# Kernel optimization log

Hardware: AMD Instinct MI355X
Metric: run time of the kernel (lower is better)

## Reference

```python
import jax, jax.numpy as jnp
import numpy as np

N = 8192       # batch_size
D = 128        # embedding dim
C = 1000       # num classes
EPS = 1e-8     # torch CosineSimilarity eps


def setup_inputs() -> dict:
    key = jax.random.key(0)
    k1, k2, k3, k4 = jax.random.split(key, 4)
    inst_embed = jax.random.normal(k1, (N, D), dtype=jnp.float32)
    proxy = jax.random.normal(k2, (N, D), dtype=jnp.float32)
    # binary mask marking same-class (non-negative) pairs, stored as float
    negative_mask = (jax.random.uniform(k3, (N, C)) < 0.5).astype(jnp.float32)
    labels = jax.random.randint(k4, (N,), 0, C)
    temperature = jnp.float32(0.07)
    margin = jnp.float32(0.0)
    return {
        'inst_embed': inst_embed,
        'proxy': proxy,
        'negative_mask': negative_mask,
        'labels': labels,
        'temperature': temperature,
        'margin': margin,
    }


def _remove_diag(M):
    # M: [h, h] -> [h, h-1], dropping the diagonal, row-major order (as torch bool-mask view)
    h = M.shape[0]
    j = jnp.arange(h - 1)[None, :]
    i = jnp.arange(h)[:, None]
    cols = j + (j >= i)  # skip column i in row i
    return jnp.take_along_axis(M, cols, axis=1)


def _l2_normalize(x):
    return x / jnp.maximum(jnp.linalg.norm(x, axis=-1, keepdims=True), EPS)


def reference(inst_embed, proxy, negative_mask, labels, temperature, margin):
    negative_mask = negative_mask.T                       # [C, N]
    xn = _l2_normalize(inst_embed)                        # [N, D]
    sim = xn @ xn.T                                       # [N, N] cosine similarity matrix
    instance_zone = jnp.exp((_remove_diag(sim) - margin) / temperature)  # [N, N-1]
    pn = _l2_normalize(proxy)
    inst2proxy_positive = jnp.exp((jnp.sum(xn * pn, axis=-1) - margin) / temperature)  # [N]
    # pos_collected_numerator == True branch
    mask_4_remove_negatives = _remove_diag(negative_mask[labels])        # [N, N-1]
    inst2inst_positives = instance_zone * mask_4_remove_negatives
    numerator = inst2proxy_positive + inst2inst_positives.sum(axis=1)
    denominator = inst2proxy_positive + instance_zone.sum(axis=1)
    criterion = -jnp.log(temperature * (numerator / denominator)).mean()
    return criterion
```

## Files before the change

kernel.cpp:

```cpp
#include <hip/hip_runtime.h>
#include <hip/hip_bf16.h>

typedef unsigned short u16;
typedef unsigned int   u32;
typedef unsigned long long u64;
typedef __attribute__((ext_vector_type(8))) short short8;
typedef __attribute__((ext_vector_type(4))) float float4v;

#define N 8192
#define D 128
#define C 1000
#define TILE 128
#define LDT 136
#define NW64 (N / 64)
#define JQ 8
#define JW (JQ * 2)
#define LOG2E 1.44269504088896340736f

__global__ void norm_kernel(const float* __restrict__ x, const float* __restrict__ pr,
                            u16* __restrict__ xnb, float* __restrict__ p_out,
                            float* __restrict__ den, float* __restrict__ num,
                            const float* __restrict__ tp, const float* __restrict__ mp) {
    const int wave = threadIdx.x >> 6;
    const int lane = threadIdx.x & 63;
    const int row  = blockIdx.x * 4 + wave;

    const float2* xr  = (const float2*)(x  + (size_t)row * D);
    const float2* prr = (const float2*)(pr + (size_t)row * D);
    float2 xv = xr[lane];
    float2 pv = prr[lane];

    float sx  = xv.x * xv.x + xv.y * xv.y;
    float sp  = pv.x * pv.x + pv.y * pv.y;
    float sxp = xv.x * pv.x + xv.y * pv.y;
    #pragma unroll
    for (int off = 32; off; off >>= 1) {
        sx  += __shfl_xor(sx,  off);
        sp  += __shfl_xor(sp,  off);
        sxp += __shfl_xor(sxp, off);
    }
    float nx = fmaxf(sqrtf(sx), 1e-8f);
    float np = fmaxf(sqrtf(sp), 1e-8f);
    float inv = 1.0f / nx;

    __hip_bfloat16 b0 = __float2bfloat16(xv.x * inv);
    __hip_bfloat16 b1 = __float2bfloat16(xv.y * inv);
    ((__hip_bfloat162*)xnb)[(size_t)row * 64 + lane] = __halves2bfloat162(b0, b1);

    if (lane == 0) {
        float T = tp[0], M = mp[0];
        p_out[row] = __expf((sxp / (nx * np) - M) / T);
        den[row] = 0.0f;
        num[row] = 0.0f;
    }
}

__global__ void pack_kernel(const float* __restrict__ nm, u64* __restrict__ packed) {
    __shared__ u32 Ls[64 * 65];
    const int lane = threadIdx.x & 63;
    const int wv   = threadIdx.x >> 6;
    const int jt   = blockIdx.x;
    const int lt   = blockIdx.y;
    const int j0   = jt * 64;
    const int l    = lt * 64 + lane;
    const bool lv  = l < C;

    #pragma unroll
    for (int rr = 0; rr < 16; rr++) {
        const int r = wv * 16 + rr;
        float v = lv ? nm[(size_t)(j0 + r) * C + l] : 0.0f;
        Ls[r * 65 + lane] = (v > 0.5f) ? 1u : 0u;
    }
    __syncthreads();
    #pragma unroll
    for (int cc = 0; cc < 16; cc++) {
        const int c = wv * 16 + cc;
        u64 m = __ballot(Ls[lane * 65 + c] != 0u);
        if (lane == 0 && (lt * 64 + c) < C)
            packed[(size_t)(lt * 64 + c) * NW64 + jt] = m;
    }
}

template <bool DIAG>
__device__ __forceinline__ void epilogue(const float4v acc[4][4], const u64* __restrict__ Ms,
                                         float dacc[4][4], float nacc[4][4],
                                         int wr, int wc, int kq, int m0,
                                         int ibase, int jbase, int q,
                                         float kA2, float kB2) {
    #pragma unroll
    for (int tm = 0; tm < 4; tm++) {
        #pragma unroll
        for (int r = 0; r < 4; r++) {
            const int lrow = wr * 64 + tm * 16 + kq * 4 + r;
            const u64 ws = Ms[lrow * JW + q * 2 + wc] >> m0;
            const u32 wlo = (u32)ws, whi = (u32)(ws >> 32);
            const int gi = ibase + lrow;
            #pragma unroll
            for (int tn = 0; tn < 4; tn++) {
                float e = __builtin_amdgcn_exp2f(fmaf(acc[tm][tn][r], kA2, kB2));
                if (DIAG) {
                    const int gj = jbase + wc * 64 + tn * 16 + m0;
                    if (gi == gj) e = 0.0f;
                }
                dacc[tm][r] += e;
                const u32 bit = ((tn < 2) ? (wlo >> (tn * 16)) : (whi >> ((tn - 2) * 16))) & 1u;
                nacc[tm][r] = fmaf((float)bit, e, nacc[tm][r]);
            }
        }
    }
}

__global__ __launch_bounds__(256, 2)
void cc_main(const u16* __restrict__ xnb, const int* __restrict__ labels,
             const u64* __restrict__ packed,
             float* __restrict__ den, float* __restrict__ num,
             const float* __restrict__ tp, const float* __restrict__ mp) {
    __shared__ u16 As[TILE * LDT];
    __shared__ u64 Ms[TILE * JW];

    const int tid  = threadIdx.x;
    const int lane = tid & 63;
    const int wv   = tid >> 6;
    const int wr   = wv >> 1;
    const int wc   = wv & 1;
    const int m0   = lane & 15;
    const int kq   = lane >> 4;
    const int ibase  = blockIdx.x * TILE;
    const int jsplit = blockIdx.y;
    const int jt0    = jsplit * JQ;

    const float T = tp[0];
    const float M = mp[0];
    const float kA2 = LOG2E / T;
    const float kB2 = -M * LOG2E / T;

    {
        const int r = tid >> 1, h = tid & 1;
        const uint4* src = (const uint4*)(xnb + (size_t)(ibase + r) * D + h * 64);
        uint4* dst = (uint4*)(As + r * LDT + h * 64);
        #pragma unroll
        for (int qq = 0; qq < 8; qq++) dst[qq] = src[qq];
    }
    #pragma unroll
    for (int t = 0; t < 8; t++) {
        const int idx = t * 256 + tid;
        const int row = idx >> 4, h = idx & 15;
        const int lab = labels[ibase + row];
        Ms[idx] = packed[(size_t)lab * NW64 + jt0 * 2 + h];
    }
    __syncthreads();

    float dacc[4][4] = {};
    float nacc[4][4] = {};

    const u16* Abase = As + (wr * 64 + m0) * LDT + kq * 8;
    const u16* Blane = xnb + (size_t)(wc * 64 + m0) * D + kq * 8;

    short8 bc[4], bn[4];
    {
        const u16* Bp = Blane + (size_t)(jt0 * TILE) * D;
        #pragma unroll
        for (int tn = 0; tn < 4; tn++) bc[tn] = *(const short8*)(Bp + tn * (16 * D));
    }

    for (int q = 0; q < JQ; q++) {
        const int jt = jt0 + q;
        const int jbase = jt * TILE;
        const u16* Bq = Blane + (size_t)jbase * D;

        float4v acc[4][4];
        #pragma unroll
        for (int a = 0; a < 4; a++)
            #pragma unroll
            for (int b = 0; b < 4; b++)
                acc[a][b] = (float4v){0.f, 0.f, 0.f, 0.f};

        #pragma unroll
        for (int kk = 0; kk < 4; kk++) {
            if (kk < 3) {
                #pragma unroll
                for (int tn = 0; tn < 4; tn++)
                    bn[tn] = *(const short8*)(Bq + tn * (16 * D) + (kk + 1) * 32);
            } else if (q < JQ - 1) {
                const u16* Bnq = Bq + (size_t)TILE * D;
                #pragma unroll
                for (int tn = 0; tn < 4; tn++)
                    bn[tn] = *(const short8*)(Bnq + tn * (16 * D));
            }
            short8 a_f[4];
            #pragma unroll
            for (int tm = 0; tm < 4; tm++)
                a_f[tm] = *(const short8*)(Abase + tm * (16 * LDT) + kk * 32);
            #pragma unroll
            for (int tm = 0; tm < 4; tm++)
                #pragma unroll
                for (int tn = 0; tn < 4; tn++)
                    acc[tm][tn] = __builtin_amdgcn_mfma_f32_16x16x32_bf16(
                        a_f[tm], bc[tn], acc[tm][tn], 0, 0, 0);
            #pragma unroll
            for (int tn = 0; tn < 4; tn++) bc[tn] = bn[tn];
        }

        if (jt == blockIdx.x)
            epilogue<true >(acc, Ms, dacc, nacc, wr, wc, kq, m0, ibase, jbase, q, kA2, kB2);
        else
            epilogue<false>(acc, Ms, dacc, nacc, wr, wc, kq, m0, ibase, jbase, q, kA2, kB2);
    }

    #pragma unroll
    for (int tm = 0; tm < 4; tm++) {
        #pragma unroll
        for (int r = 0; r < 4; r++) {
            float d = dacc[tm][r], n = nacc[tm][r];
            #pragma unroll
            for (int off = 1; off < 16; off <<= 1) {
                d += __shfl_xor(d, off);
                n += __shfl_xor(n, off);
            }
            if (m0 == 0) {
                const int gi = ibase + wr * 64 + tm * 16 + kq * 4 + r;
                atomicAdd(&den[gi], d);
                atomicAdd(&num[gi], n);
            }
        }
    }
}

__global__ void loss_kernel(const float* __restrict__ p, const float* __restrict__ den,
                            const float* __restrict__ num, float* __restrict__ out,
                            const float* __restrict__ tp) {
    __shared__ float red[16];
    const float T = tp[0];
    float s = 0.0f;
    #pragma unroll
    for (int t = 0; t < N / 1024; t++) {
        const int i = t * 1024 + threadIdx.x;
        float pi = p[i];
        s += -__logf(T * (pi + num[i]) / (pi + den[i]));
    }
    #pragma unroll
    for (int off = 32; off; off >>= 1) s += __shfl_xor(s, off);
    const int lane = threadIdx.x & 63, wv = threadIdx.x >> 6;
    if (lane == 0) red[wv] = s;
    __syncthreads();
    if (wv == 0) {
        float t = (lane < 16) ? red[lane] : 0.0f;
        #pragma unroll
        for (int off = 8; off; off >>= 1) t += __shfl_xor(t, off);
        if (lane == 0) out[0] = t / (float)N;
    }
}

extern "C" void kernel_launch(void* const* d_in, const int* in_sizes, int n_in,
                              void* d_out, int out_size, void* d_ws, size_t ws_size,
                              hipStream_t stream) {
    (void)in_sizes; (void)n_in; (void)out_size; (void)ws_size;
    const float* inst   = (const float*)d_in[0];
    const float* proxy  = (const float*)d_in[1];
    const float* nm     = (const float*)d_in[2];
    const int*   labels = (const int*)d_in[3];
    const float* temp   = (const float*)d_in[4];
    const float* marg   = (const float*)d_in[5];
    float* out = (float*)d_out;

    char* ws = (char*)d_ws;
    u16*   xnb    = (u16*)ws;
    float* p_arr  = (float*)(ws + 2097152);
    u64*   packed = (u64*)(ws + 2129920);
    float* den    = (float*)(ws + 3153920);
    float* num    = (float*)(ws + 3186688);

    pack_kernel<<<dim3(N / 64, 16), 256, 0, stream>>>(nm, packed);
    norm_kernel<<<N / 4, 256, 0, stream>>>(inst, proxy, xnb, p_arr, den, num, temp, marg);
    cc_main<<<dim3(N / TILE, 8), 256, 0, stream>>>(xnb, labels, packed, den, num, temp, marg);
    loss_kernel<<<1, 1024, 0, stream>>>(p_arr, den, num, out, temp);
}
```

Before: 142.4 us.

## Fuse prep kernels, fold loss into main kernel via last-block counter, vectorize epilogue

Merges the mask-packing and normalization kernels into one launch split by block index. The separate loss kernel is removed: the last cc_main block to finish, found with an atomic counter, computes the final reduction. The epilogue now works on float4 vectors per row group so the exp and accumulate steps can issue as packed operations. Together these cut launch overhead and the tail launch, at the cost of an atomic counter, a threadfence in every block, and a serial reduction done by one block.

```diff
diff --git a/kernel.cpp b/kernel.cpp
--- a/kernel.cpp
+++ b/kernel.cpp
@@ -15,97 +15,113 @@
 #define NW64 (N / 64)
 #define JQ 8
 #define JW (JQ * 2)
+#define NBLK (64 * 8)
 #define LOG2E 1.44269504088896340736f
 
-__global__ void norm_kernel(const float* __restrict__ x, const float* __restrict__ pr,
+__global__ void prep_kernel(const float* __restrict__ nm, u64* __restrict__ packed,
+                            const float* __restrict__ x, const float* __restrict__ pr,
                             u16* __restrict__ xnb, float* __restrict__ p_out,
                             float* __restrict__ den, float* __restrict__ num,
+                            u32* __restrict__ counter,
                             const float* __restrict__ tp, const float* __restrict__ mp) {
-    const int wave = threadIdx.x >> 6;
-    const int lane = threadIdx.x & 63;
-    const int row  = blockIdx.x * 4 + wave;
-
-    const float2* xr  = (const float2*)(x  + (size_t)row * D);
-    const float2* prr = (const float2*)(pr + (size_t)row * D);
-    float2 xv = xr[lane];
-    float2 pv = prr[lane];
-
-    float sx  = xv.x * xv.x + xv.y * xv.y;
-    float sp  = pv.x * pv.x + pv.y * pv.y;
-    float sxp = xv.x * pv.x + xv.y * pv.y;
-    #pragma unroll
-    for (int off = 32; off; off >>= 1) {
-        sx  += __shfl_xor(sx,  off);
-        sp  += __shfl_xor(sp,  off);
-        sxp += __shfl_xor(sxp, off);
-    }
-    float nx = fmaxf(sqrtf(sx), 1e-8f);
-    float np = fmaxf(sqrtf(sp), 1e-8f);
-    float inv = 1.0f / nx;
-
-    __hip_bfloat16 b0 = __float2bfloat16(xv.x * inv);
-    __hip_bfloat16 b1 = __float2bfloat16(xv.y * inv);
-    ((__hip_bfloat162*)xnb)[(size_t)row * 64 + lane] = __halves2bfloat162(b0, b1);
-
-    if (lane == 0) {
-        float T = tp[0], M = mp[0];
-        p_out[row] = __expf((sxp / (nx * np) - M) / T);
-        den[row] = 0.0f;
-        num[row] = 0.0f;
-    }
-}
-
-__global__ void pack_kernel(const float* __restrict__ nm, u64* __restrict__ packed) {
     __shared__ u32 Ls[64 * 65];
+    const int bid  = blockIdx.x;
     const int lane = threadIdx.x & 63;
     const int wv   = threadIdx.x >> 6;
-    const int jt   = blockIdx.x;
-    const int lt   = blockIdx.y;
-    const int j0   = jt * 64;
-    const int l    = lt * 64 + lane;
-    const bool lv  = l < C;
-
-    #pragma unroll
-    for (int rr = 0; rr < 16; rr++) {
-        const int r = wv * 16 + rr;
-        float v = lv ? nm[(size_t)(j0 + r) * C + l] : 0.0f;
-        Ls[r * 65 + lane] = (v > 0.5f) ? 1u : 0u;
-    }
-    __syncthreads();
-    #pragma unroll
-    for (int cc = 0; cc < 16; cc++) {
-        const int c = wv * 16 + cc;
-        u64 m = __ballot(Ls[lane * 65 + c] != 0u);
-        if (lane == 0 && (lt * 64 + c) < C)
-            packed[(size_t)(lt * 64 + c) * NW64 + jt] = m;
+
+    if (bid < 2048) {
+        const int jt = bid & 127;
+        const int lt = bid >> 7;
+        const int j0 = jt * 64;
+        const int l  = lt * 64 + lane;
+        const bool lv = l < C;
+        if (bid == 0 && threadIdx.x == 0) counter[0] = 0u;
+
+        #pragma unroll
+        for (int rr = 0; rr < 16; rr++) {
+            const int r = wv * 16 + rr;
+            float v = lv ? nm[(size_t)(j0 + r) * C + l] : 0.0f;
+            Ls[r * 65 + lane] = (v > 0.5f) ? 1u : 0u;
+        }
+        __syncthreads();
+        #pragma unroll
+        for (int cc = 0; cc < 16; cc++) {
+            const int c = wv * 16 + cc;
+            u64 m = __ballot(Ls[lane * 65 + c] != 0u);
+            if (lane == 0 && (lt * 64 + c) < C)
+                packed[(size_t)(lt * 64 + c) * NW64 + jt] = m;
+        }
+    } else {
+        const int row = (bid - 2048) * 4 + wv;
+        const float2* xr  = (const float2*)(x  + (size_t)row * D);
+        const float2* prr = (const float2*)(pr + (size_t)row * D);
+        float2 xv = xr[lane];
+        float2 pv = prr[lane];
+
+        float sx  = xv.x * xv.x + xv.y * xv.y;
+        float sp  = pv.x * pv.x + pv.y * pv.y;
+        float sxp = xv.x * pv.x + xv.y * pv.y;
+        #pragma unroll
+        for (int off = 32; off; off >>= 1) {
+            sx  += __shfl_xor(sx,  off);
+            sp  += __shfl_xor(sp,  off);
+            sxp += __shfl_xor(sxp, off);
+        }
+        float nx = fmaxf(sqrtf(sx), 1e-8f);
+        float np = fmaxf(sqrtf(sp), 1e-8f);
+        float inv = 1.0f / nx;
+
+        __hip_bfloat16 b0 = __float2bfloat16(xv.x * inv);
+        __hip_bfloat16 b1 = __float2bfloat16(xv.y * inv);
+        ((__hip_bfloat162*)xnb)[(size_t)row * 64 + lane] = __halves2bfloat162(b0, b1);
+
+        if (lane == 0) {
+            float T = tp[0], M = mp[0];
+            p_out[row] = __expf((sxp / (nx * np) - M) / T);
+            den[row] = 0.0f;
+            num[row] = 0.0f;
+        }
     }
 }
 
 template <bool DIAG>
 __device__ __forceinline__ void epilogue(const float4v acc[4][4], const u64* __restrict__ Ms,
-                                         float dacc[4][4], float nacc[4][4],
+                                         float4v dacc[4], float4v nacc[4],
                                          int wr, int wc, int kq, int m0,
                                          int ibase, int jbase, int q,
                                          float kA2, float kB2) {
     #pragma unroll
     for (int tm = 0; tm < 4; tm++) {
+        u32 lo[4], hi[4];
         #pragma unroll
         for (int r = 0; r < 4; r++) {
             const int lrow = wr * 64 + tm * 16 + kq * 4 + r;
-            const u64 ws = Ms[lrow * JW + q * 2 + wc] >> m0;
-            const u32 wlo = (u32)ws, whi = (u32)(ws >> 32);
-            const int gi = ibase + lrow;
-            #pragma unroll
-            for (int tn = 0; tn < 4; tn++) {
-                float e = __builtin_amdgcn_exp2f(fmaf(acc[tm][tn][r], kA2, kB2));
-                if (DIAG) {
-                    const int gj = jbase + wc * 64 + tn * 16 + m0;
-                    if (gi == gj) e = 0.0f;
+            const u64 w = Ms[lrow * JW + q * 2 + wc];
+            lo[r] = (u32)(w >> m0);
+            hi[r] = (u32)(w >> (m0 + 32));
+        }
+        #pragma unroll
+        for (int tn = 0; tn < 4; tn++) {
+            float4v t = acc[tm][tn] * kA2 + kB2;
+            float4v e;
+            #pragma unroll
+            for (int r = 0; r < 4; r++) e[r] = __builtin_amdgcn_exp2f(t[r]);
+            if (DIAG) {
+                const int gj = jbase + wc * 64 + tn * 16 + m0;
+                #pragma unroll
+                for (int r = 0; r < 4; r++) {
+                    const int gi = ibase + wr * 64 + tm * 16 + kq * 4 + r;
+                    if (gi == gj) e[r] = 0.0f;
                 }
-                dacc[tm][r] += e;
-                const u32 bit = ((tn < 2) ? (wlo >> (tn * 16)) : (whi >> ((tn - 2) * 16))) & 1u;
-                nacc[tm][r] = fmaf((float)bit, e, nacc[tm][r]);
-            }
+            }
+            dacc[tm] += e;
+            float4v mf;
+            #pragma unroll
+            for (int r = 0; r < 4; r++) {
+                const u32 bit = ((tn < 2) ? (lo[r] >> (tn * 16)) : (hi[r] >> ((tn - 2) * 16))) & 1u;
+                mf[r] = (float)bit;
+            }
+            nacc[tm] += mf * e;
         }
     }
 }
@@ -114,9 +130,13 @@
 void cc_main(const u16* __restrict__ xnb, const int* __restrict__ labels,
              const u64* __restrict__ packed,
              float* __restrict__ den, float* __restrict__ num,
+             const float* __restrict__ p_arr, u32* __restrict__ counter,
+             float* __restrict__ out,
              const float* __restrict__ tp, const float* __restrict__ mp) {
     __shared__ u16 As[TILE * LDT];
     __shared__ u64 Ms[TILE * JW];
+    __shared__ u32 done_s;
+    __shared__ float red[4];
 
     const int tid  = threadIdx.x;
     const int lane = tid & 63;
@@ -150,8 +170,8 @@
     }
     __syncthreads();
 
-    float dacc[4][4] = {};
-    float nacc[4][4] = {};
+    float4v dacc[4] = {};
+    float4v nacc[4] = {};
 
     const u16* Abase = As + (wr * 64 + m0) * LDT + kq * 8;
     const u16* Blane = xnb + (size_t)(wc * 64 + m0) * D + kq * 8;
@@ -224,30 +244,30 @@
             }
         }
     }
-}
-
-__global__ void loss_kernel(const float* __restrict__ p, const float* __restrict__ den,
-                            const float* __restrict__ num, float* __restrict__ out,
-                            const float* __restrict__ tp) {
-    __shared__ float red[16];
-    const float T = tp[0];
-    float s = 0.0f;
-    #pragma unroll
-    for (int t = 0; t < N / 1024; t++) {
-        const int i = t * 1024 + threadIdx.x;
-        float pi = p[i];
-        s += -__logf(T * (pi + num[i]) / (pi + den[i]));
-    }
-    #pragma unroll
-    for (int off = 32; off; off >>= 1) s += __shfl_xor(s, off);
-    const int lane = threadIdx.x & 63, wv = threadIdx.x >> 6;
-    if (lane == 0) red[wv] = s;
+
+    __threadfence();
+    if (tid == 0) done_s = atomicAdd(counter, 1u);
     __syncthreads();
-    if (wv == 0) {
-        float t = (lane < 16) ? red[lane] : 0.0f;
-        #pragma unroll
-        for (int off = 8; off; off >>= 1) t += __shfl_xor(t, off);
-        if (lane == 0) out[0] = t / (float)N;
+    if (done_s == NBLK - 1) {
+        float s = 0.0f;
+        #pragma unroll
+        for (int t = 0; t < N / 256; t++) {
+            const int i = t * 256 + tid;
+            float dv = __hip_atomic_load(&den[i], __ATOMIC_RELAXED, __HIP_MEMORY_SCOPE_AGENT);
+            float nv = __hip_atomic_load(&num[i], __ATOMIC_RELAXED, __HIP_MEMORY_SCOPE_AGENT);
+            float pi = p_arr[i];
+            s += -__logf(T * (pi + nv) / (pi + dv));
+        }
+        #pragma unroll
+        for (int off = 32; off; off >>= 1) s += __shfl_xor(s, off);
+        if (lane == 0) red[wv] = s;
+        __syncthreads();
+        if (wv == 0) {
+            float tt = (lane < 4) ? red[lane] : 0.0f;
+            tt += __shfl_xor(tt, 1);
+            tt += __shfl_xor(tt, 2);
+            if (lane == 0) out[0] = tt / (float)N;
+        }
     }
 }
 
@@ -269,9 +289,10 @@
     u64*   packed = (u64*)(ws + 2129920);
     float* den    = (float*)(ws + 3153920);
     float* num    = (float*)(ws + 3186688);
-
-    pack_kernel<<<dim3(N / 64, 16), 256, 0, stream>>>(nm, packed);
-    norm_kernel<<<N / 4, 256, 0, stream>>>(inst, proxy, xnb, p_arr, den, num, temp, marg);
-    cc_main<<<dim3(N / TILE, 8), 256, 0, stream>>>(xnb, labels, packed, den, num, temp, marg);
-    loss_kernel<<<1, 1024, 0, stream>>>(p_arr, den, num, out, temp);
-}
+    u32*   cnt    = (u32*)(ws + 3219456);
+
+    prep_kernel<<<4096, 256, 0, stream>>>(nm, packed, inst, proxy, xnb, p_arr,
+                                          den, num, cnt, temp, marg);
+    cc_main<<<dim3(N / TILE, 8), 256, 0, stream>>>(xnb, labels, packed, den, num,
+                                                   p_arr, cnt, out, temp, marg);
+}
```

Measured after the change: 164.2 us. +15.4%, slower.
